# Kernel tuning notes

Measured on AMD Instinct MI355X. Metric: run time of the kernel, lower is better.

## Reference

```python
import jax, jax.numpy as jnp
import numpy as np

D_MODEL = 1024
N_HEADS = 16
D_K = 64
D_FF = 4096
B = 8
S = 1024
NEG = -1e32
EPS = 1e-5


def _layer_norm(x, g, b):
    mu = jnp.mean(x, axis=-1, keepdims=True)
    var = jnp.var(x, axis=-1, keepdims=True)
    return (x - mu) * jax.lax.rsqrt(var + EPS) * g + b


def setup_inputs() -> dict:
    key = jax.random.key(0)
    ks = jax.random.split(key, 16)
    sc = 0.02
    inp = {
        'x': jax.random.normal(ks[0], (B, S, D_MODEL), dtype=jnp.float32),
        'Wq': jax.random.normal(ks[1], (D_MODEL, D_MODEL), jnp.float32) * sc,
        'bq': jnp.zeros((D_MODEL,), jnp.float32),
        'Wk': jax.random.normal(ks[2], (D_MODEL, D_MODEL), jnp.float32) * sc,
        'bk': jnp.zeros((D_MODEL,), jnp.float32),
        'Wv': jax.random.normal(ks[3], (D_MODEL, D_MODEL), jnp.float32) * sc,
        'bv': jnp.zeros((D_MODEL,), jnp.float32),
        'Wo': jax.random.normal(ks[4], (D_MODEL, D_MODEL), jnp.float32) * sc,
        'bo': jnp.zeros((D_MODEL,), jnp.float32),
        'W1': jax.random.normal(ks[5], (D_MODEL, D_FF), jnp.float32) * sc,
        'b1': jnp.zeros((D_FF,), jnp.float32),
        'W2': jax.random.normal(ks[6], (D_FF, D_MODEL), jnp.float32) * sc,
        'b2': jnp.zeros((D_MODEL,), jnp.float32),
        'g1': jnp.ones((D_MODEL,), jnp.float32),
        'beta1': jnp.zeros((D_MODEL,), jnp.float32),
        'g3': jnp.ones((D_MODEL,), jnp.float32),
        'beta3': jnp.zeros((D_MODEL,), jnp.float32),
    }
    return inp


def _block(x, Wq, bq, Wk, bk, Wv, bv, Wo, bo, W1, b1, W2, b2, g1, beta1, g3, beta3):
    bs, seqlen, _ = x.shape
    # QKV projections -> [b, h, s, d_k]
    def split_heads(t):
        return t.reshape(bs, seqlen, N_HEADS, D_K).transpose(0, 2, 1, 3)
    q = split_heads(x @ Wq + bq)
    k = split_heads(x @ Wk + bk)
    v = split_heads(x @ Wv + bv)
    # scores [b,h,s,s]
    scores = jnp.einsum('bhqd,bhkd->bhqk', q, k) / jnp.sqrt(jnp.float32(D_K))
    # mask=0 case: src_mask = (triu(ones, k=0) == 0) -> allow strictly lower (j < i)
    i = jnp.arange(seqlen)[:, None]
    j = jnp.arange(seqlen)[None, :]
    allowed = (j < i)  # [s, s]
    scores = jnp.where(allowed[None, None], scores, NEG)
    attn = jax.nn.softmax(scores, axis=-1)
    # zero_pad: zero out the first query row of attention probs
    attn = attn * (i > 0).astype(attn.dtype)[None, None]
    ctx = jnp.einsum('bhqk,bhkd->bhqd', attn, v)  # [b,h,s,d_k]
    concat = ctx.transpose(0, 2, 1, 3).reshape(bs, seqlen, D_MODEL)
    attn_out = concat @ Wo + bo
    # residual + LN (dropout p=0)
    h1 = _layer_norm(x + attn_out, g1, beta1)
    # position-wise FFN
    ffn = jax.nn.relu(h1 @ W1 + b1) @ W2 + b2
    out = _layer_norm(h1 + ffn, g3, beta3)
    return out


def reference(x, Wq, bq, Wk, bk, Wv, bv, Wo, bo, W1, b1, W2, b2, g1, beta1, g3, beta3):
    return _block(x, Wq, bq, Wk, bk, Wv, bv, Wo, bo, W1, b1, W2, b2, g1, beta1, g3, beta3)
```

## Files before the change

### kernel.cpp

```cpp
#include <hip/hip_runtime.h>
#include <hip/hip_bf16.h>

typedef __bf16 bf16x8 __attribute__((ext_vector_type(8)));
typedef __bf16 bf16x4 __attribute__((ext_vector_type(4)));
typedef float f32x4 __attribute__((ext_vector_type(4)));

#define GLOBAL_LOAD_LDS16(gp, lp)                                              \
  __builtin_amdgcn_global_load_lds(                                            \
      (const __attribute__((address_space(1))) void*)(gp),                     \
      (__attribute__((address_space(3))) void*)(lp), 16, 0, 0)

__global__ __launch_bounds__(256) void transpose4_f2b_k(
    const float* __restrict__ s0, const float* __restrict__ s1,
    const float* __restrict__ s2, const float* __restrict__ s3,
    __bf16* __restrict__ dst) {
  __shared__ float tile[32][33];
  const float* srcs[4] = {s0, s1, s2, s3};
  const float* src = srcs[blockIdx.z];
  __bf16* d = dst + ((size_t)blockIdx.z << 20);
  const int bx = blockIdx.x * 32, by = blockIdx.y * 32;
  const int tx = threadIdx.x & 31, ty = threadIdx.x >> 5;
#pragma unroll
  for (int i = 0; i < 32; i += 8)
    tile[ty + i][tx] = src[(size_t)(by + ty + i) * 1024 + bx + tx];
  __syncthreads();
#pragma unroll
  for (int i = 0; i < 32; i += 8)
    d[(size_t)(bx + ty + i) * 1024 + by + tx] = (__bf16)tile[tx][ty + i];
}

__global__ __launch_bounds__(256) void transpose_f2b_k(
    const float* __restrict__ src, __bf16* __restrict__ dst, int R, int C) {
  __shared__ float tile[32][33];
  const int bx = blockIdx.x * 32, by = blockIdx.y * 32;
  const int tx = threadIdx.x & 31, ty = threadIdx.x >> 5;
#pragma unroll
  for (int i = 0; i < 32; i += 8)
    tile[ty + i][tx] = src[(size_t)(by + ty + i) * C + bx + tx];
  __syncthreads();
#pragma unroll
  for (int i = 0; i < 32; i += 8)
    dst[(size_t)(bx + ty + i) * R + by + tx] = (__bf16)tile[tx][ty + i];
}

__global__ __launch_bounds__(256) void transpose_v_k(
    const __bf16* __restrict__ src, __bf16* __restrict__ dst) {
  __shared__ __bf16 tile[32][33];
  const int bh = blockIdx.z;
  const int s0 = blockIdx.x * 32, d0 = blockIdx.y * 32;
  const size_t base = (size_t)bh << 16;
  const int tx = threadIdx.x & 31, ty = threadIdx.x >> 5;
#pragma unroll
  for (int i = 0; i < 32; i += 8)
    tile[ty + i][tx] = src[base + (size_t)(s0 + ty + i) * 64 + d0 + tx];
  __syncthreads();
#pragma unroll
  for (int i = 0; i < 32; i += 8)
    dst[base + (size_t)(d0 + ty + i) * 1024 + s0 + tx] = tile[tx][ty + i];
}

__global__ __launch_bounds__(256) void convert_f2b_k(const float* __restrict__ s,
                                                     __bf16* __restrict__ d) {
  const size_t i = ((size_t)blockIdx.x * 256 + threadIdx.x) * 4;
  const float4 v = *(const float4*)(s + i);
  bf16x4 o;
  o[0] = (__bf16)v.x; o[1] = (__bf16)v.y; o[2] = (__bf16)v.z; o[3] = (__bf16)v.w;
  *(bf16x4*)(d + i) = o;
}

__global__ void concat3_k(const float* a, const float* b, const float* c,
                          float* o) {
  int i = blockIdx.x * 256 + threadIdx.x;
  if (i < 1024) o[i] = a[i];
  else if (i < 2048) o[i] = b[i - 1024];
  else if (i < 3072) o[i] = c[i - 2048];
}

template <int EPI>
__global__ __launch_bounds__(256) void gemm_bt(const __bf16* __restrict__ A,
                                               const __bf16* __restrict__ Bt,
                                               const float* __restrict__ bias,
                                               __bf16* __restrict__ C,
                                               int M, int N, int K) {
  __shared__ __align__(16) __bf16 As[128 * 32];
  __shared__ __align__(16) __bf16 Bs[128 * 32];
  const int tid = threadIdx.x;
  const int wave = tid >> 6, lane = tid & 63;
  const int quad = lane >> 4, l15 = lane & 15;
  const int wm = wave >> 1, wn = wave & 1;
  const int m0 = blockIdx.x * 128, n0 = blockIdx.y * 128;
  const int rsub = lane >> 2;
  const int kch = lane & 3;

  f32x4 acc[4][4] = {};

  for (int k0 = 0; k0 < K; k0 += 32) {
#pragma unroll
    for (int j = 0; j < 2; ++j) {
      const int rg = (wave * 2 + j) * 16 + rsub;
      GLOBAL_LOAD_LDS16(A + (size_t)(m0 + rg) * K + k0 + kch * 8,
                        As + (wave * 2 + j) * 512);
      GLOBAL_LOAD_LDS16(Bt + (size_t)(n0 + rg) * K + k0 + kch * 8,
                        Bs + (wave * 2 + j) * 512);
    }
    __syncthreads();
    bf16x8 af[4], bfr[4];
#pragma unroll
    for (int mt = 0; mt < 4; ++mt)
      af[mt] = *(const bf16x8*)(As + (wm * 64 + mt * 16 + l15) * 32 + quad * 8);
#pragma unroll
    for (int nt = 0; nt < 4; ++nt)
      bfr[nt] = *(const bf16x8*)(Bs + (wn * 64 + nt * 16 + l15) * 32 + quad * 8);
#pragma unroll
    for (int mt = 0; mt < 4; ++mt)
#pragma unroll
      for (int nt = 0; nt < 4; ++nt)
        acc[mt][nt] = __builtin_amdgcn_mfma_f32_16x16x32_bf16(
            af[mt], bfr[nt], acc[mt][nt], 0, 0, 0);
    __syncthreads();
  }

#pragma unroll
  for (int nt = 0; nt < 4; ++nt) {
    const int col = n0 + wn * 64 + nt * 16 + l15;
    const float bv = bias[col];
#pragma unroll
    for (int mt = 0; mt < 4; ++mt) {
#pragma unroll
      for (int r = 0; r < 4; ++r) {
        const int row = m0 + wm * 64 + mt * 16 + quad * 4 + r;
        float v = acc[mt][nt][r] + bv;
        if (EPI == 1) v = fmaxf(v, 0.0f);
        size_t oidx;
        if (EPI == 2) {
          const int which = col >> 10, wi = col & 1023;
          const int h = wi >> 6, d = wi & 63;
          const int b = row >> 10, s = row & 1023;
          oidx = ((size_t)which << 23) +
                 (((size_t)(b * 16 + h) << 16) + s * 64 + d);
        } else {
          oidx = (size_t)row * N + col;
        }
        C[oidx] = (__bf16)v;
      }
    }
  }
}

__global__ __launch_bounds__(256) void gemm_bt64(const __bf16* __restrict__ A,
                                                 const __bf16* __restrict__ Bt,
                                                 const float* __restrict__ bias,
                                                 __bf16* __restrict__ C,
                                                 int M, int N, int K) {
  __shared__ __align__(16) __bf16 As[128 * 64];
  __shared__ __align__(16) __bf16 Bs[64 * 64];
  const int tid = threadIdx.x;
  const int wave = tid >> 6, lane = tid & 63;
  const int quad = lane >> 4, l15 = lane & 15;
  const int wm = wave >> 1, wn = wave & 1;
  const int m0 = blockIdx.x * 128, n0 = blockIdx.y * 64;
  const int srow = tid >> 3;
  const int sch = tid & 7;

  f32x4 acc[4][2] = {};

  for (int k0 = 0; k0 < K; k0 += 64) {
#pragma unroll
    for (int p = 0; p < 4; ++p) {
      const int row = p * 32 + srow;
      GLOBAL_LOAD_LDS16(A + (size_t)(m0 + row) * K + k0 + ((sch ^ (row & 7)) * 8),
                        As + p * 2048 + wave * 512);
    }
#pragma unroll
    for (int p = 0; p < 2; ++p) {
      const int row = p * 32 + srow;
      GLOBAL_LOAD_LDS16(Bt + (size_t)(n0 + row) * K + k0 + ((sch ^ (row & 7)) * 8),
                        Bs + p * 2048 + wave * 512);
    }
    __syncthreads();
    bf16x8 af[4][2], bfr[2][2];
#pragma unroll
    for (int kk = 0; kk < 2; ++kk) {
#pragma unroll
      for (int mt = 0; mt < 4; ++mt) {
        const int row = wm * 64 + mt * 16 + l15;
        af[mt][kk] =
            *(const bf16x8*)(As + row * 64 + (((kk * 4 + quad) ^ (row & 7)) * 8));
      }
#pragma unroll
      for (int nt = 0; nt < 2; ++nt) {
        const int row = wn * 32 + nt * 16 + l15;
        bfr[nt][kk] =
            *(const bf16x8*)(Bs + row * 64 + (((kk * 4 + quad) ^ (row & 7)) * 8));
      }
    }
#pragma unroll
    for (int kk = 0; kk < 2; ++kk)
#pragma unroll
      for (int mt = 0; mt < 4; ++mt)
#pragma unroll
        for (int nt = 0; nt < 2; ++nt)
          acc[mt][nt] = __builtin_amdgcn_mfma_f32_16x16x32_bf16(
              af[mt][kk], bfr[nt][kk], acc[mt][nt], 0, 0, 0);
    __syncthreads();
  }

#pragma unroll
  for (int nt = 0; nt < 2; ++nt) {
    const int col = n0 + wn * 32 + nt * 16 + l15;
    const float bv = bias[col];
#pragma unroll
    for (int mt = 0; mt < 4; ++mt) {
#pragma unroll
      for (int r = 0; r < 4; ++r) {
        const int row = m0 + wm * 64 + mt * 16 + quad * 4 + r;
        C[(size_t)row * N + col] = (__bf16)(acc[mt][nt][r] + bv);
      }
    }
  }
}

__global__ __launch_bounds__(256) void attn_kernel(const __bf16* __restrict__ Q,
                                                   const __bf16* __restrict__ Kg,
                                                   const __bf16* __restrict__ Vt,
                                                   __bf16* __restrict__ ctx) {
  const int qp = blockIdx.x;
  const int bh = blockIdx.y;
  const int b = bh >> 4, h = bh & 15;
  const int tid = threadIdx.x, wave = tid >> 6, lane = tid & 63;
  const int quad = lane >> 4, l15 = lane & 15;
  const size_t hoff = (size_t)bh << 16;
  const __bf16* Qh = Q + hoff;
  const __bf16* Kh = Kg + hoff;
  const __bf16* Vh = Vt + hoff;

  __shared__ __align__(16) __bf16 Ks[64 * 64];
  __shared__ __align__(16) __bf16 Vs[64 * 64];
  __shared__ __align__(16) __bf16 Ps[4][32 * 72];
  __shared__ float lL[128];

  const int skey = wave * 8 + (lane >> 3);
  const int sgr = lane & 7;

#pragma unroll
  for (int pass = 0; pass < 2; ++pass) {
    const int qt = pass ? (7 - qp) : qp;
    const int qb = qt * 128;

    bf16x8 qf[2][2];
#pragma unroll
    for (int g = 0; g < 2; ++g) {
      const int qrow = qb + wave * 32 + g * 16 + l15;
      bf16x8 t0 = *(const bf16x8*)(Qh + (size_t)qrow * 64 + quad * 8);
      bf16x8 t1 = *(const bf16x8*)(Qh + (size_t)qrow * 64 + 32 + quad * 8);
#pragma unroll
      for (int e = 0; e < 8; ++e) {
        qf[g][0][e] = (__bf16)((float)t0[e] * 0.125f);
        qf[g][1][e] = (__bf16)((float)t1[e] * 0.125f);
      }
    }

    f32x4 oacc[4][2] = {};
    float lrun[2][4] = {};

    const int ktmax = 2 * qt + 1;
    for (int kt = 0; kt <= ktmax; ++kt) {
      __syncthreads();
#pragma unroll
      for (int j = 0; j < 2; ++j) {
        const int row = skey + 32 * j;
        GLOBAL_LOAD_LDS16(
            Kh + (size_t)(kt * 64 + row) * 64 + ((sgr ^ (row & 7)) * 8),
            Ks + j * 2048 + wave * 512);
        GLOBAL_LOAD_LDS16(
            Vh + (size_t)row * 1024 + kt * 64 + ((sgr ^ (row & 7)) * 8),
            Vs + j * 2048 + wave * 512);
      }
      __syncthreads();

      f32x4 sacc[2][4] = {};
#pragma unroll
      for (int nt = 0; nt < 4; ++nt) {
        const int key = nt * 16 + l15, sw = key & 7;
        bf16x8 kf0 = *(const bf16x8*)(Ks + key * 64 + ((quad ^ sw) * 8));
        bf16x8 kf1 = *(const bf16x8*)(Ks + key * 64 + (((quad + 4) ^ sw) * 8));
#pragma unroll
        for (int g = 0; g < 2; ++g) {
          sacc[g][nt] = __builtin_amdgcn_mfma_f32_16x16x32_bf16(
              qf[g][0], kf0, sacc[g][nt], 0, 0, 0);
          sacc[g][nt] = __builtin_amdgcn_mfma_f32_16x16x32_bf16(
              qf[g][1], kf1, sacc[g][nt], 0, 0, 0);
        }
      }

      const bool tilemask = (kt >= 2 * qt);
#pragma unroll
      for (int g = 0; g < 2; ++g)
#pragma unroll
        for (int nt = 0; nt < 4; ++nt) {
          const int key = kt * 64 + nt * 16 + l15;
#pragma unroll
          for (int r = 0; r < 4; ++r) {
            float p = __expf(fminf(sacc[g][nt][r], 60.0f));
            if (tilemask && key >= qb + wave * 32 + g * 16 + quad * 4 + r)
              p = 0.0f;
            sacc[g][nt][r] = p;
            lrun[g][r] += p;
          }
        }

#pragma unroll
      for (int g = 0; g < 2; ++g)
#pragma unroll
        for (int nt = 0; nt < 4; ++nt)
#pragma unroll
          for (int r = 0; r < 4; ++r)
            Ps[wave][(g * 16 + quad * 4 + r) * 72 + nt * 16 + l15] =
                (__bf16)sacc[g][nt][r];

#pragma unroll
      for (int kc = 0; kc < 2; ++kc) {
        bf16x8 pf[2];
#pragma unroll
        for (int g = 0; g < 2; ++g)
          pf[g] = *(const bf16x8*)(&Ps[wave][(g * 16 + l15) * 72 + kc * 32 +
                                             quad * 8]);
#pragma unroll
        for (int mdt = 0; mdt < 4; ++mdt) {
          const int d = mdt * 16 + l15, sw = d & 7;
          bf16x8 vf =
              *(const bf16x8*)(Vs + d * 64 + (((kc * 4 + quad) ^ sw) * 8));
#pragma unroll
          for (int g = 0; g < 2; ++g)
            oacc[mdt][g] = __builtin_amdgcn_mfma_f32_16x16x32_bf16(
                vf, pf[g], oacc[mdt][g], 0, 0, 0);
        }
      }
    }

#pragma unroll
    for (int g = 0; g < 2; ++g)
#pragma unroll
      for (int r = 0; r < 4; ++r) {
        float s = lrun[g][r];
#pragma unroll
        for (int d = 1; d < 16; d <<= 1) s += __shfl_xor(s, d);
        if (l15 == 0) lL[wave * 32 + g * 16 + quad * 4 + r] = s;
      }
    float linv[2];
#pragma unroll
    for (int g = 0; g < 2; ++g) {
      const float l = lL[wave * 32 + g * 16 + l15];
      linv[g] = (qb + wave * 32 + g * 16 + l15 == 0) ? 0.0f : (1.0f / l);
    }
    __bf16* Ot = Ps[wave];
#pragma unroll
    for (int mdt = 0; mdt < 4; ++mdt)
#pragma unroll
      for (int g = 0; g < 2; ++g)
#pragma unroll
        for (int r = 0; r < 4; ++r)
          Ot[(g * 16 + l15) * 72 + mdt * 16 + quad * 4 + r] =
              (__bf16)(oacc[mdt][g][r] * linv[g]);
#pragma unroll
    for (int rr = 0; rr < 2; ++rr)
#pragma unroll
      for (int j = 0; j < 2; ++j) {
        const int row = rr * 16 + (lane >> 2), chk = (lane & 3) + 4 * j;
        bf16x8 ov = *(const bf16x8*)(Ot + row * 72 + chk * 8);
        const size_t oi = ((size_t)(b * 1024 + qb + wave * 32 + row)) * 1024 +
                          h * 64 + chk * 8;
        *(bf16x8*)(ctx + oi) = ov;
      }
  }
}

template <typename TX, typename TY, typename TO>
__global__ __launch_bounds__(256) void add_ln_kernel(const TX* __restrict__ x,
                                                     const TY* __restrict__ y,
                                                     const float* __restrict__ g,
                                                     const float* __restrict__ be,
                                                     TO* __restrict__ out) {
  const int row = blockIdx.x;
  const size_t base = (size_t)row * 1024;
  const int t = threadIdx.x;
  float xv[4], yv[4];
  if constexpr (sizeof(TX) == 4) {
    const float4 a = *(const float4*)(x + base + t * 4);
    xv[0] = a.x; xv[1] = a.y; xv[2] = a.z; xv[3] = a.w;
  } else {
    const bf16x4 a = *(const bf16x4*)(x + base + t * 4);
#pragma unroll
    for (int i = 0; i < 4; ++i) xv[i] = (float)a[i];
  }
  if constexpr (sizeof(TY) == 4) {
    const float4 a = *(const float4*)(y + base + t * 4);
    yv[0] = a.x; yv[1] = a.y; yv[2] = a.z; yv[3] = a.w;
  } else {
    const bf16x4 a = *(const bf16x4*)(y + base + t * 4);
#pragma unroll
    for (int i = 0; i < 4; ++i) yv[i] = (float)a[i];
  }
  float v[4], s = 0.0f, s2 = 0.0f;
#pragma unroll
  for (int i = 0; i < 4; ++i) {
    v[i] = xv[i] + yv[i];
    s += v[i];
    s2 += v[i] * v[i];
  }
#pragma unroll
  for (int m = 1; m < 64; m <<= 1) {
    s += __shfl_xor(s, m);
    s2 += __shfl_xor(s2, m);
  }
  __shared__ float ss[4], ss2[4];
  const int w = t >> 6;
  if ((t & 63) == 0) { ss[w] = s; ss2[w] = s2; }
  __syncthreads();
  s = ss[0] + ss[1] + ss[2] + ss[3];
  s2 = ss2[0] + ss2[1] + ss2[2] + ss2[3];
  const float mu = s * (1.0f / 1024.0f);
  const float var = s2 * (1.0f / 1024.0f) - mu * mu;
  const float rstd = rsqrtf(var + 1e-5f);
#pragma unroll
  for (int i = 0; i < 4; ++i) {
    const float o = (v[i] - mu) * rstd * g[t * 4 + i] + be[t * 4 + i];
    out[base + t * 4 + i] = (TO)o;
  }
}

extern "C" void kernel_launch(void* const* d_in, const int* in_sizes, int n_in,
                              void* d_out, int out_size, void* d_ws,
                              size_t ws_size, hipStream_t stream) {
  (void)in_sizes; (void)n_in; (void)out_size; (void)ws_size;
  const float* x   = (const float*)d_in[0];
  const float* Wq  = (const float*)d_in[1];
  const float* bq  = (const float*)d_in[2];
  const float* Wk  = (const float*)d_in[3];
  const float* bk  = (const float*)d_in[4];
  const float* Wv  = (const float*)d_in[5];
  const float* bv  = (const float*)d_in[6];
  const float* Wo  = (const float*)d_in[7];
  const float* bo  = (const float*)d_in[8];
  const float* W1  = (const float*)d_in[9];
  const float* b1  = (const float*)d_in[10];
  const float* W2  = (const float*)d_in[11];
  const float* b2  = (const float*)d_in[12];
  const float* g1  = (const float*)d_in[13];
  const float* be1 = (const float*)d_in[14];
  const float* g3  = (const float*)d_in[15];
  const float* be3 = (const float*)d_in[16];

  char* ws = (char*)d_ws;
  __bf16* Qb    = (__bf16*)(ws + 0);
  __bf16* Kb    = (__bf16*)(ws + (16u << 20));
  __bf16* Vb    = (__bf16*)(ws + (32u << 20));
  __bf16* ctx   = (__bf16*)(ws + (48u << 20));
  __bf16* mid   = (__bf16*)(ws + 0);
  __bf16* aout  = (__bf16*)(ws + (64u << 20));
  __bf16* h1    = aout;
  __bf16* xb    = (__bf16*)(ws + (80u << 20));
  __bf16* Vtb   = (__bf16*)(ws + (80u << 20));
  __bf16* fout  = (__bf16*)(ws + (80u << 20));
  __bf16* WqkvT = (__bf16*)(ws + (96u << 20));
  __bf16* WoT   = (__bf16*)(ws + (96u << 20) + 3 * (1u << 21));
  __bf16* W1T   = (__bf16*)(ws + (104u << 20));
  __bf16* W2T   = (__bf16*)(ws + (112u << 20));
  float*  bqkv  = (float*)(ws + (120u << 20));
  float*  outp  = (float*)d_out;

  const dim3 blk(256);
  convert_f2b_k<<<dim3(8192), blk, 0, stream>>>(x, xb);
  transpose4_f2b_k<<<dim3(32, 32, 4), blk, 0, stream>>>(Wq, Wk, Wv, Wo, WqkvT);
  transpose_f2b_k<<<dim3(128, 32), blk, 0, stream>>>(W1, W1T, 1024, 4096);
  transpose_f2b_k<<<dim3(32, 128), blk, 0, stream>>>(W2, W2T, 4096, 1024);
  concat3_k<<<dim3(12), blk, 0, stream>>>(bq, bk, bv, bqkv);

  gemm_bt<2><<<dim3(64, 24), blk, 0, stream>>>(xb, WqkvT, bqkv, Qb, 8192, 3072, 1024);
  transpose_v_k<<<dim3(32, 2, 128), blk, 0, stream>>>(Vb, Vtb);
  attn_kernel<<<dim3(4, 128), blk, 0, stream>>>(Qb, Kb, Vtb, ctx);
  gemm_bt64<<<dim3(64, 16), blk, 0, stream>>>(ctx, WoT, bo, aout, 8192, 1024, 1024);
  add_ln_kernel<float, __bf16, __bf16><<<dim3(8192), blk, 0, stream>>>(
      x, aout, g1, be1, h1);
  gemm_bt<1><<<dim3(64, 32), blk, 0, stream>>>(h1, W1T, b1, mid, 8192, 4096, 1024);
  gemm_bt64<<<dim3(64, 16), blk, 0, stream>>>(mid, W2T, b2, fout, 8192, 1024, 4096);
  add_ln_kernel<__bf16, __bf16, float><<<dim3(8192), blk, 0, stream>>>(
      h1, fout, g3, be3, outp);
}
```

Baseline: 521.2 us.

## Use 8 waves of 16 query rows in attention and reorder GEMM epilogue stores

The attention kernel now launches 512 threads (8 waves), with each wave owning 16 query rows instead of 32. Each thread issues one K and one V async load per tile instead of two, and the per-wave masking condition is recomputed at the new granularity. This gives more waves per block to hide latency and fewer registers per wave, at the cost of reloading each K/V fragment from LDS for half as many rows. Separately, both GEMM epilogues hoist the bias loads and iterate over columns innermost, so neighbouring stores sit in the same row.

Result: no change. 531.4 us (+2.0%).

```diff
diff --git a/kernel.cpp b/kernel.cpp
--- a/kernel.cpp
+++ b/kernel.cpp
@@ -120,16 +120,18 @@
     __syncthreads();
   }
 
-#pragma unroll
-  for (int nt = 0; nt < 4; ++nt) {
-    const int col = n0 + wn * 64 + nt * 16 + l15;
-    const float bv = bias[col];
-#pragma unroll
-    for (int mt = 0; mt < 4; ++mt) {
-#pragma unroll
-      for (int r = 0; r < 4; ++r) {
-        const int row = m0 + wm * 64 + mt * 16 + quad * 4 + r;
-        float v = acc[mt][nt][r] + bv;
+  float bv[4];
+#pragma unroll
+  for (int nt = 0; nt < 4; ++nt) bv[nt] = bias[n0 + wn * 64 + nt * 16 + l15];
+#pragma unroll
+  for (int mt = 0; mt < 4; ++mt) {
+#pragma unroll
+    for (int r = 0; r < 4; ++r) {
+      const int row = m0 + wm * 64 + mt * 16 + quad * 4 + r;
+#pragma unroll
+      for (int nt = 0; nt < 4; ++nt) {
+        const int col = n0 + wn * 64 + nt * 16 + l15;
+        float v = acc[mt][nt][r] + bv[nt];
         if (EPI == 1) v = fmaxf(v, 0.0f);
         size_t oidx;
         if (EPI == 2) {
@@ -205,22 +207,24 @@
     __syncthreads();
   }
 
-#pragma unroll
-  for (int nt = 0; nt < 2; ++nt) {
-    const int col = n0 + wn * 32 + nt * 16 + l15;
-    const float bv = bias[col];
-#pragma unroll
-    for (int mt = 0; mt < 4; ++mt) {
-#pragma unroll
-      for (int r = 0; r < 4; ++r) {
-        const int row = m0 + wm * 64 + mt * 16 + quad * 4 + r;
-        C[(size_t)row * N + col] = (__bf16)(acc[mt][nt][r] + bv);
-      }
-    }
-  }
-}
-
-__global__ __launch_bounds__(256) void attn_kernel(const __bf16* __restrict__ Q,
+  float bv[2];
+#pragma unroll
+  for (int nt = 0; nt < 2; ++nt) bv[nt] = bias[n0 + wn * 32 + nt * 16 + l15];
+#pragma unroll
+  for (int mt = 0; mt < 4; ++mt) {
+#pragma unroll
+    for (int r = 0; r < 4; ++r) {
+      const int row = m0 + wm * 64 + mt * 16 + quad * 4 + r;
+#pragma unroll
+      for (int nt = 0; nt < 2; ++nt) {
+        const int col = n0 + wn * 32 + nt * 16 + l15;
+        C[(size_t)row * N + col] = (__bf16)(acc[mt][nt][r] + bv[nt]);
+      }
+    }
+  }
+}
+
+__global__ __launch_bounds__(512) void attn_kernel(const __bf16* __restrict__ Q,
                                                    const __bf16* __restrict__ Kg,
                                                    const __bf16* __restrict__ Vt,
                                                    __bf16* __restrict__ ctx) {
@@ -236,10 +240,10 @@
 
   __shared__ __align__(16) __bf16 Ks[64 * 64];
   __shared__ __align__(16) __bf16 Vs[64 * 64];
-  __shared__ __align__(16) __bf16 Ps[4][32 * 72];
+  __shared__ __align__(16) __bf16 Ps[8][16 * 72];
   __shared__ float lL[128];
 
-  const int skey = wave * 8 + (lane >> 3);
+  const int srow = wave * 8 + (lane >> 3);
   const int sgr = lane & 7;
 
 #pragma unroll
@@ -247,131 +251,102 @@
     const int qt = pass ? (7 - qp) : qp;
     const int qb = qt * 128;
 
-    bf16x8 qf[2][2];
-#pragma unroll
-    for (int g = 0; g < 2; ++g) {
-      const int qrow = qb + wave * 32 + g * 16 + l15;
+    bf16x8 qf[2];
+    {
+      const int qrow = qb + wave * 16 + l15;
       bf16x8 t0 = *(const bf16x8*)(Qh + (size_t)qrow * 64 + quad * 8);
       bf16x8 t1 = *(const bf16x8*)(Qh + (size_t)qrow * 64 + 32 + quad * 8);
 #pragma unroll
       for (int e = 0; e < 8; ++e) {
-        qf[g][0][e] = (__bf16)((float)t0[e] * 0.125f);
-        qf[g][1][e] = (__bf16)((float)t1[e] * 0.125f);
-      }
-    }
-
-    f32x4 oacc[4][2] = {};
-    float lrun[2][4] = {};
+        qf[0][e] = (__bf16)((float)t0[e] * 0.125f);
+        qf[1][e] = (__bf16)((float)t1[e] * 0.125f);
+      }
+    }
+
+    f32x4 oacc[4] = {};
+    float lrun[4] = {};
 
     const int ktmax = 2 * qt + 1;
     for (int kt = 0; kt <= ktmax; ++kt) {
       __syncthreads();
-#pragma unroll
-      for (int j = 0; j < 2; ++j) {
-        const int row = skey + 32 * j;
-        GLOBAL_LOAD_LDS16(
-            Kh + (size_t)(kt * 64 + row) * 64 + ((sgr ^ (row & 7)) * 8),
-            Ks + j * 2048 + wave * 512);
-        GLOBAL_LOAD_LDS16(
-            Vh + (size_t)row * 1024 + kt * 64 + ((sgr ^ (row & 7)) * 8),
-            Vs + j * 2048 + wave * 512);
-      }
+      GLOBAL_LOAD_LDS16(
+          Kh + (size_t)(kt * 64 + srow) * 64 + ((sgr ^ (srow & 7)) * 8),
+          Ks + wave * 512);
+      GLOBAL_LOAD_LDS16(
+          Vh + (size_t)srow * 1024 + kt * 64 + ((sgr ^ (srow & 7)) * 8),
+          Vs + wave * 512);
       __syncthreads();
 
-      f32x4 sacc[2][4] = {};
+      f32x4 sacc[4] = {};
 #pragma unroll
       for (int nt = 0; nt < 4; ++nt) {
         const int key = nt * 16 + l15, sw = key & 7;
         bf16x8 kf0 = *(const bf16x8*)(Ks + key * 64 + ((quad ^ sw) * 8));
         bf16x8 kf1 = *(const bf16x8*)(Ks + key * 64 + (((quad + 4) ^ sw) * 8));
-#pragma unroll
-        for (int g = 0; g < 2; ++g) {
-          sacc[g][nt] = __builtin_amdgcn_mfma_f32_16x16x32_bf16(
-              qf[g][0], kf0, sacc[g][nt], 0, 0, 0);
-          sacc[g][nt] = __builtin_amdgcn_mfma_f32_16x16x32_bf16(
-              qf[g][1], kf1, sacc[g][nt], 0, 0, 0);
+        sacc[nt] = __builtin_amdgcn_mfma_f32_16x16x32_bf16(qf[0], kf0,
+                                                           sacc[nt], 0, 0, 0);
+        sacc[nt] = __builtin_amdgcn_mfma_f32_16x16x32_bf16(qf[1], kf1,
+                                                           sacc[nt], 0, 0, 0);
+      }
+
+      const bool tilemask = (kt * 64 + 63 >= qb + wave * 16);
+#pragma unroll
+      for (int nt = 0; nt < 4; ++nt) {
+        const int key = kt * 64 + nt * 16 + l15;
+#pragma unroll
+        for (int r = 0; r < 4; ++r) {
+          float p = __expf(fminf(sacc[nt][r], 60.0f));
+          if (tilemask && key >= qb + wave * 16 + quad * 4 + r) p = 0.0f;
+          sacc[nt][r] = p;
+          lrun[r] += p;
         }
       }
 
-      const bool tilemask = (kt >= 2 * qt);
-#pragma unroll
-      for (int g = 0; g < 2; ++g)
-#pragma unroll
-        for (int nt = 0; nt < 4; ++nt) {
-          const int key = kt * 64 + nt * 16 + l15;
-#pragma unroll
-          for (int r = 0; r < 4; ++r) {
-            float p = __expf(fminf(sacc[g][nt][r], 60.0f));
-            if (tilemask && key >= qb + wave * 32 + g * 16 + quad * 4 + r)
-              p = 0.0f;
-            sacc[g][nt][r] = p;
-            lrun[g][r] += p;
-          }
-        }
-
-#pragma unroll
-      for (int g = 0; g < 2; ++g)
-#pragma unroll
-        for (int nt = 0; nt < 4; ++nt)
-#pragma unroll
-          for (int r = 0; r < 4; ++r)
-            Ps[wave][(g * 16 + quad * 4 + r) * 72 + nt * 16 + l15] =
-                (__bf16)sacc[g][nt][r];
+#pragma unroll
+      for (int nt = 0; nt < 4; ++nt)
+#pragma unroll
+        for (int r = 0; r < 4; ++r)
+          Ps[wave][(quad * 4 + r) * 72 + nt * 16 + l15] = (__bf16)sacc[nt][r];
 
 #pragma unroll
       for (int kc = 0; kc < 2; ++kc) {
-        bf16x8 pf[2];
-#pragma unroll
-        for (int g = 0; g < 2; ++g)
-          pf[g] = *(const bf16x8*)(&Ps[wave][(g * 16 + l15) * 72 + kc * 32 +
-                                             quad * 8]);
+        bf16x8 pf =
+            *(const bf16x8*)(&Ps[wave][l15 * 72 + kc * 32 + quad * 8]);
 #pragma unroll
         for (int mdt = 0; mdt < 4; ++mdt) {
           const int d = mdt * 16 + l15, sw = d & 7;
           bf16x8 vf =
               *(const bf16x8*)(Vs + d * 64 + (((kc * 4 + quad) ^ sw) * 8));
-#pragma unroll
-          for (int g = 0; g < 2; ++g)
-            oacc[mdt][g] = __builtin_amdgcn_mfma_f32_16x16x32_bf16(
-                vf, pf[g], oacc[mdt][g], 0, 0, 0);
+          oacc[mdt] = __builtin_amdgcn_mfma_f32_16x16x32_bf16(vf, pf,
+                                                              oacc[mdt], 0, 0, 0);
         }
       }
     }
 
 #pragma unroll
-    for (int g = 0; g < 2; ++g)
-#pragma unroll
-      for (int r = 0; r < 4; ++r) {
-        float s = lrun[g][r];
-#pragma unroll
-        for (int d = 1; d < 16; d <<= 1) s += __shfl_xor(s, d);
-        if (l15 == 0) lL[wave * 32 + g * 16 + quad * 4 + r] = s;
-      }
-    float linv[2];
-#pragma unroll
-    for (int g = 0; g < 2; ++g) {
-      const float l = lL[wave * 32 + g * 16 + l15];
-      linv[g] = (qb + wave * 32 + g * 16 + l15 == 0) ? 0.0f : (1.0f / l);
-    }
+    for (int r = 0; r < 4; ++r) {
+      float s = lrun[r];
+#pragma unroll
+      for (int d = 1; d < 16; d <<= 1) s += __shfl_xor(s, d);
+      if (l15 == 0) lL[wave * 16 + quad * 4 + r] = s;
+    }
+    const float l = lL[wave * 16 + l15];
+    const float linv = (qb + wave * 16 + l15 == 0) ? 0.0f : (1.0f / l);
+
     __bf16* Ot = Ps[wave];
 #pragma unroll
     for (int mdt = 0; mdt < 4; ++mdt)
 #pragma unroll
-      for (int g = 0; g < 2; ++g)
-#pragma unroll
-        for (int r = 0; r < 4; ++r)
-          Ot[(g * 16 + l15) * 72 + mdt * 16 + quad * 4 + r] =
-              (__bf16)(oacc[mdt][g][r] * linv[g]);
-#pragma unroll
-    for (int rr = 0; rr < 2; ++rr)
-#pragma unroll
-      for (int j = 0; j < 2; ++j) {
-        const int row = rr * 16 + (lane >> 2), chk = (lane & 3) + 4 * j;
-        bf16x8 ov = *(const bf16x8*)(Ot + row * 72 + chk * 8);
-        const size_t oi = ((size_t)(b * 1024 + qb + wave * 32 + row)) * 1024 +
-                          h * 64 + chk * 8;
-        *(bf16x8*)(ctx + oi) = ov;
-      }
+      for (int r = 0; r < 4; ++r)
+        Ot[l15 * 72 + mdt * 16 + quad * 4 + r] = (__bf16)(oacc[mdt][r] * linv);
+#pragma unroll
+    for (int j = 0; j < 2; ++j) {
+      const int row = lane >> 2, chk = (lane & 3) + 4 * j;
+      bf16x8 ov = *(const bf16x8*)(Ot + row * 72 + chk * 8);
+      const size_t oi = ((size_t)(b * 1024 + qb + wave * 16 + row)) * 1024 +
+                        h * 64 + chk * 8;
+      *(bf16x8*)(ctx + oi) = ov;
+    }
   }
 }
 
@@ -478,7 +453,7 @@
 
   gemm_bt<2><<<dim3(64, 24), blk, 0, stream>>>(xb, WqkvT, bqkv, Qb, 8192, 3072, 1024);
   transpose_v_k<<<dim3(32, 2, 128), blk, 0, stream>>>(Vb, Vtb);
-  attn_kernel<<<dim3(4, 128), blk, 0, stream>>>(Qb, Kb, Vtb, ctx);
+  attn_kernel<<<dim3(4, 128), dim3(512), 0, stream>>>(Qb, Kb, Vtb, ctx);
   gemm_bt64<<<dim3(64, 16), blk, 0, stream>>>(ctx, WoT, bo, aout, 8192, 1024, 1024);
   add_ln_kernel<float, __bf16, __bf16><<<dim3(8192), blk, 0, stream>>>(
       x, aout, g1, be1, h1);
```

## Switch 128x128 GEMM to 32x32x16 MFMA with 64-wide K tiles and swizzled LDS

Applied to the files above, without the earlier changes.

Rewrites the QKV and FFN1 GEMM kernel to use 32x32x16 bf16 MFMA tiles instead of 16x16x32, doubles the K step to 64, and applies an XOR swizzle to LDS rows to avoid bank conflicts. The larger MFMA shape cuts LDS fragment reads per FLOP, and the wider K step halves the number of barriers. It also reorders the epilogue loops in gemm_bt64 so the bias is loaded once per column tile. The cost is higher register pressure from the 16-wide accumulators and double the LDS footprint, which may reduce occupancy.

Measured after the change: 481.9 us. -7.5%, faster.

```diff
diff --git a/kernel.cpp b/kernel.cpp
--- a/kernel.cpp
+++ b/kernel.cpp
@@ -4,6 +4,7 @@
 typedef __bf16 bf16x8 __attribute__((ext_vector_type(8)));
 typedef __bf16 bf16x4 __attribute__((ext_vector_type(4)));
 typedef float f32x4 __attribute__((ext_vector_type(4)));
+typedef float f32x16 __attribute__((ext_vector_type(16)));
 
 #define GLOBAL_LOAD_LDS16(gp, lp)                                              \
   __builtin_amdgcn_global_load_lds(                                            \
@@ -77,59 +78,71 @@
 }
 
 template <int EPI>
-__global__ __launch_bounds__(256) void gemm_bt(const __bf16* __restrict__ A,
-                                               const __bf16* __restrict__ Bt,
-                                               const float* __restrict__ bias,
-                                               __bf16* __restrict__ C,
-                                               int M, int N, int K) {
-  __shared__ __align__(16) __bf16 As[128 * 32];
-  __shared__ __align__(16) __bf16 Bs[128 * 32];
+__global__ __launch_bounds__(256) void gemm_bt32(const __bf16* __restrict__ A,
+                                                 const __bf16* __restrict__ Bt,
+                                                 const float* __restrict__ bias,
+                                                 __bf16* __restrict__ C,
+                                                 int M, int N, int K) {
+  __shared__ __align__(16) __bf16 As[128 * 64];
+  __shared__ __align__(16) __bf16 Bs[128 * 64];
   const int tid = threadIdx.x;
   const int wave = tid >> 6, lane = tid & 63;
-  const int quad = lane >> 4, l15 = lane & 15;
+  const int l31 = lane & 31, hi = lane >> 5;
   const int wm = wave >> 1, wn = wave & 1;
   const int m0 = blockIdx.x * 128, n0 = blockIdx.y * 128;
-  const int rsub = lane >> 2;
-  const int kch = lane & 3;
-
-  f32x4 acc[4][4] = {};
-
-  for (int k0 = 0; k0 < K; k0 += 32) {
-#pragma unroll
-    for (int j = 0; j < 2; ++j) {
-      const int rg = (wave * 2 + j) * 16 + rsub;
-      GLOBAL_LOAD_LDS16(A + (size_t)(m0 + rg) * K + k0 + kch * 8,
-                        As + (wave * 2 + j) * 512);
-      GLOBAL_LOAD_LDS16(Bt + (size_t)(n0 + rg) * K + k0 + kch * 8,
-                        Bs + (wave * 2 + j) * 512);
+  const int srsub = lane >> 3;
+  const int sch = lane & 7;
+
+  f32x16 acc[2][2] = {};
+
+  for (int k0 = 0; k0 < K; k0 += 64) {
+#pragma unroll
+    for (int p = 0; p < 4; ++p) {
+      const int g = wave * 4 + p;
+      const int row = g * 8 + srsub;
+      GLOBAL_LOAD_LDS16(A + (size_t)(m0 + row) * K + k0 + ((sch ^ (row & 7)) * 8),
+                        As + g * 512);
+      GLOBAL_LOAD_LDS16(Bt + (size_t)(n0 + row) * K + k0 + ((sch ^ (row & 7)) * 8),
+                        Bs + g * 512);
     }
     __syncthreads();
-    bf16x8 af[4], bfr[4];
-#pragma unroll
-    for (int mt = 0; mt < 4; ++mt)
-      af[mt] = *(const bf16x8*)(As + (wm * 64 + mt * 16 + l15) * 32 + quad * 8);
-#pragma unroll
-    for (int nt = 0; nt < 4; ++nt)
-      bfr[nt] = *(const bf16x8*)(Bs + (wn * 64 + nt * 16 + l15) * 32 + quad * 8);
-#pragma unroll
-    for (int mt = 0; mt < 4; ++mt)
-#pragma unroll
-      for (int nt = 0; nt < 4; ++nt)
-        acc[mt][nt] = __builtin_amdgcn_mfma_f32_16x16x32_bf16(
-            af[mt], bfr[nt], acc[mt][nt], 0, 0, 0);
+#pragma unroll
+    for (int kk = 0; kk < 4; ++kk) {
+      bf16x8 af[2], bf[2];
+#pragma unroll
+      for (int mt = 0; mt < 2; ++mt) {
+        const int row = wm * 64 + mt * 32 + l31;
+        af[mt] = *(const bf16x8*)(As + row * 64 +
+                                  (((kk * 2 + hi) ^ (row & 7)) * 8));
+      }
+#pragma unroll
+      for (int nt = 0; nt < 2; ++nt) {
+        const int row = wn * 64 + nt * 32 + l31;
+        bf[nt] = *(const bf16x8*)(Bs + row * 64 +
+                                  (((kk * 2 + hi) ^ (row & 7)) * 8));
+      }
+#pragma unroll
+      for (int mt = 0; mt < 2; ++mt)
+#pragma unroll
+        for (int nt = 0; nt < 2; ++nt)
+          acc[mt][nt] = __builtin_amdgcn_mfma_f32_32x32x16_bf16(
+              af[mt], bf[nt], acc[mt][nt], 0, 0, 0);
+    }
     __syncthreads();
   }
 
-#pragma unroll
-  for (int nt = 0; nt < 4; ++nt) {
-    const int col = n0 + wn * 64 + nt * 16 + l15;
-    const float bv = bias[col];
-#pragma unroll
-    for (int mt = 0; mt < 4; ++mt) {
-#pragma unroll
-      for (int r = 0; r < 4; ++r) {
-        const int row = m0 + wm * 64 + mt * 16 + quad * 4 + r;
-        float v = acc[mt][nt][r] + bv;
+  float bvv[2];
+#pragma unroll
+  for (int nt = 0; nt < 2; ++nt) bvv[nt] = bias[n0 + wn * 64 + nt * 32 + l31];
+#pragma unroll
+  for (int mt = 0; mt < 2; ++mt) {
+#pragma unroll
+    for (int i = 0; i < 16; ++i) {
+      const int row = m0 + wm * 64 + mt * 32 + (i & 3) + 8 * (i >> 2) + 4 * hi;
+#pragma unroll
+      for (int nt = 0; nt < 2; ++nt) {
+        const int col = n0 + wn * 64 + nt * 32 + l31;
+        float v = acc[mt][nt][i] + bvv[nt];
         if (EPI == 1) v = fmaxf(v, 0.0f);
         size_t oidx;
         if (EPI == 2) {
@@ -205,16 +218,18 @@
     __syncthreads();
   }
 
-#pragma unroll
-  for (int nt = 0; nt < 2; ++nt) {
-    const int col = n0 + wn * 32 + nt * 16 + l15;
-    const float bv = bias[col];
-#pragma unroll
-    for (int mt = 0; mt < 4; ++mt) {
-#pragma unroll
-      for (int r = 0; r < 4; ++r) {
-        const int row = m0 + wm * 64 + mt * 16 + quad * 4 + r;
-        C[(size_t)row * N + col] = (__bf16)(acc[mt][nt][r] + bv);
+  float bv[2];
+#pragma unroll
+  for (int nt = 0; nt < 2; ++nt) bv[nt] = bias[n0 + wn * 32 + nt * 16 + l15];
+#pragma unroll
+  for (int mt = 0; mt < 4; ++mt) {
+#pragma unroll
+    for (int r = 0; r < 4; ++r) {
+      const int row = m0 + wm * 64 + mt * 16 + quad * 4 + r;
+#pragma unroll
+      for (int nt = 0; nt < 2; ++nt) {
+        const int col = n0 + wn * 32 + nt * 16 + l15;
+        C[(size_t)row * N + col] = (__bf16)(acc[mt][nt][r] + bv[nt]);
       }
     }
   }
@@ -476,13 +491,13 @@
   transpose_f2b_k<<<dim3(32, 128), blk, 0, stream>>>(W2, W2T, 4096, 1024);
   concat3_k<<<dim3(12), blk, 0, stream>>>(bq, bk, bv, bqkv);
 
-  gemm_bt<2><<<dim3(64, 24), blk, 0, stream>>>(xb, WqkvT, bqkv, Qb, 8192, 3072, 1024);
+  gemm_bt32<2><<<dim3(64, 24), blk, 0, stream>>>(xb, WqkvT, bqkv, Qb, 8192, 3072, 1024);
   transpose_v_k<<<dim3(32, 2, 128), blk, 0, stream>>>(Vb, Vtb);
   attn_kernel<<<dim3(4, 128), blk, 0, stream>>>(Qb, Kb, Vtb, ctx);
   gemm_bt64<<<dim3(64, 16), blk, 0, stream>>>(ctx, WoT, bo, aout, 8192, 1024, 1024);
   add_ln_kernel<float, __bf16, __bf16><<<dim3(8192), blk, 0, stream>>>(
       x, aout, g1, be1, h1);
-  gemm_bt<1><<<dim3(64, 32), blk, 0, stream>>>(h1, W1T, b1, mid, 8192, 4096, 1024);
+  gemm_bt32<1><<<dim3(64, 32), blk, 0, stream>>>(h1, W1T, b1, mid, 8192, 4096, 1024);
   gemm_bt64<<<dim3(64, 16), blk, 0, stream>>>(mid, W2T, b2, fout, 8192, 1024, 4096);
   add_ln_kernel<__bf16, __bf16, float><<<dim3(8192), blk, 0, stream>>>(
       h1, fout, g3, be3, outp);
```
